# Kernel optimization log

Hardware: AMD Instinct MI355X
Metric: run time of the kernel (lower is better)

## Reference

```python
import jax, jax.numpy as jnp
import numpy as np

EPS = 1e-12  # matches torch F.normalize default eps

def _l2_normalize(v, axis=-1):
    n = jnp.sqrt(jnp.sum(v * v, axis=axis, keepdims=True))
    return v / jnp.maximum(n, EPS)

def setup_inputs() -> dict:
    key = jax.random.key(0)
    k1, k2, k3 = jax.random.split(key, 3)
    B, S, D_IN, D_OUT, T = 4, 4096, 1024, 1024, 1024
    std = 1.0 / np.sqrt(D_IN)
    return {
        "x": jax.random.normal(k1, (B, S, D_IN), dtype=jnp.float32),
        "key_tokens": jax.random.normal(k2, (T, D_IN), dtype=jnp.float32) * std,
        "value_tokens": jax.random.normal(k3, (T, D_OUT), dtype=jnp.float32) * std,
        "temp": jnp.ones((T, 1), dtype=jnp.float32),
    }

def reference(x, key_tokens, value_tokens, temp):
    # x: [B,S,D_in]; key_tokens: [T,D_in]; value_tokens: [T,D_out]; temp: [T,1]
    x_norm = _l2_normalize(x)                      # [B,S,D_in]
    k_norm = _l2_normalize(key_tokens)             # [T,D_in]
    sim = jnp.einsum('bsd,td->bst', x_norm, k_norm)  # [B,S,T]
    sim = sim * jax.nn.sigmoid(temp).reshape(1, 1, -1)
    # mod_softmax: scale each row to RMS-norm sqrt(T), then exact GELU
    T = sim.shape[-1]
    scale = jnp.sqrt(jnp.float32(T)) / jnp.sqrt(jnp.sum(sim * sim, axis=-1, keepdims=True))
    weights = jax.nn.gelu(sim * scale, approximate=False)  # [B,S,T]
    return jnp.einsum('bst,to->bso', weights, value_tokens)  # [B,S,D_out]
```

## Files before the change

### kernel.cpp

```cpp
#include <hip/hip_runtime.h>
#include <math.h>

typedef __attribute__((ext_vector_type(8))) short short8;
typedef __attribute__((ext_vector_type(4))) float floatx4;

__device__ __forceinline__ float bf2f(unsigned short u) {
    union { unsigned int u; float f; } v;
    v.u = ((unsigned int)u) << 16;
    return v.f;
}

__device__ __forceinline__ unsigned short f2bf(float f) {
    union { float f; unsigned int u; } v;
    v.f = f;
    unsigned int r = v.u + 0x7fffu + ((v.u >> 16) & 1u);
    return (unsigned short)(r >> 16);
}

__device__ __forceinline__ void gload16_lds(const void* g, void* l) {
    __builtin_amdgcn_global_load_lds(
        (const __attribute__((address_space(1))) unsigned int*)g,
        (__attribute__((address_space(3))) unsigned int*)l, 16, 0, 0);
}

__global__ __launch_bounds__(256) void prep_kernel(
    const float* __restrict__ x, const float* __restrict__ key,
    const float* __restrict__ temp, const float* __restrict__ val,
    unsigned short* __restrict__ xb, unsigned short* __restrict__ kf,
    unsigned short* __restrict__ VT, float* __restrict__ rowsq,
    int M, int T, int D, int Dout) {
    const int bid = blockIdx.x;
    const int t = threadIdx.x;
    __shared__ float ls[4];
    __shared__ float facs;
    __shared__ unsigned short tile[64][65];

    if (bid < M + T) {
        const bool isx = bid < M;
        const int row = isx ? bid : bid - M;
        const float* src = isx ? (x + (size_t)row * D) : (key + (size_t)row * D);
        float4 v = ((const float4*)src)[t];
        float s = v.x * v.x + v.y * v.y + v.z * v.z + v.w * v.w;
#pragma unroll
        for (int o = 32; o > 0; o >>= 1) s += __shfl_xor(s, o, 64);
        if ((t & 63) == 0) ls[t >> 6] = s;
        __syncthreads();
        if (t == 0) {
            float tot = ls[0] + ls[1] + ls[2] + ls[3];
            float inv = 1.0f / fmaxf(sqrtf(tot), 1e-12f);
            if (isx) {
                facs = inv;
                rowsq[row] = 0.0f;
            } else {
                float tf = temp[row];
                facs = inv / (1.0f + expf(-tf));
            }
        }
        __syncthreads();
        const float fa = facs;
        ushort4 o4;
        o4.x = f2bf(v.x * fa); o4.y = f2bf(v.y * fa);
        o4.z = f2bf(v.z * fa); o4.w = f2bf(v.w * fa);
        unsigned short* dst = isx ? (xb + (size_t)row * D) : (kf + (size_t)row * D);
        ((ushort4*)dst)[t] = o4;
    } else {
        const int idx = bid - M - T;
        const int nCt = Dout >> 6;
        const int c0 = (idx % nCt) * 64;
        const int r0 = (idx / nCt) * 64;
        for (int i = t; i < 4096; i += 256) {
            int r = i >> 6, c = i & 63;
            tile[r][c] = f2bf(val[(size_t)(r0 + r) * Dout + c0 + c]);
        }
        __syncthreads();
        for (int i = t; i < 4096; i += 256) {
            int r = i >> 6, c = i & 63;
            VT[(size_t)(c0 + r) * T + r0 + c] = tile[c][r];
        }
    }
}

template <int MODE>
__global__ __launch_bounds__(256) void gemm_bt(const unsigned short* __restrict__ A,
                                               const unsigned short* __restrict__ B,
                                               void* __restrict__ Cv,
                                               float* __restrict__ rowsq,
                                               int M, int N, int K) {
    __shared__ __align__(16) unsigned short As[128 * 64];
    __shared__ __align__(16) unsigned short Bs[128 * 64];
    const int tid = threadIdx.x;
    const int lane = tid & 63;
    const int w = tid >> 6;
    const int m0 = blockIdx.x * 128;
    const int n0 = blockIdx.y * 128;
    const int wm = (w & 1) * 64;
    const int wn = (w >> 1) * 64;
    const int cl = lane & 15;
    const int q = lane >> 4;

    floatx4 acc[4][4];
#pragma unroll
    for (int i = 0; i < 4; i++)
#pragma unroll
        for (int j = 0; j < 4; j++) acc[i][j] = (floatx4){0.f, 0.f, 0.f, 0.f};

    const int srow = tid >> 2;
    const int skof = (tid & 3) * 8;
    const unsigned short* ga0 = A + (size_t)(m0 + srow) * K + skof;
    const unsigned short* ga1 = A + (size_t)(m0 + srow + 64) * K + skof;
    const unsigned short* gb0 = B + (size_t)(n0 + srow) * K + skof;
    const unsigned short* gb1 = B + (size_t)(n0 + srow + 64) * K + skof;
    unsigned short* la0 = &As[(w * 64) * 8];
    unsigned short* la1 = &As[(256 + w * 64) * 8];
    unsigned short* lb0 = &Bs[(w * 64) * 8];
    unsigned short* lb1 = &Bs[(256 + w * 64) * 8];

    const int a_off = (wm + cl) * 32 + q * 8;
    const int b_off = (wn + cl) * 32 + q * 8;

    for (int kt = 0; kt < K; kt += 64) {
        __syncthreads();
#pragma unroll
        for (int h = 0; h < 2; h++) {
            const int go = kt + h * 32;
            const int lo = h * 4096;
            gload16_lds(ga0 + go, la0 + lo);
            gload16_lds(ga1 + go, la1 + lo);
            gload16_lds(gb0 + go, lb0 + lo);
            gload16_lds(gb1 + go, lb1 + lo);
        }
        __syncthreads();
#pragma unroll
        for (int h = 0; h < 2; h++) {
            const int lo = h * 4096;
            short8 af[4], bfr[4];
#pragma unroll
            for (int mt = 0; mt < 4; mt++)
                af[mt] = *(const short8*)&As[lo + a_off + mt * 16 * 32];
#pragma unroll
            for (int nt = 0; nt < 4; nt++)
                bfr[nt] = *(const short8*)&Bs[lo + b_off + nt * 16 * 32];
#pragma unroll
            for (int mt = 0; mt < 4; mt++)
#pragma unroll
                for (int nt = 0; nt < 4; nt++)
                    acc[mt][nt] = __builtin_amdgcn_mfma_f32_16x16x32_bf16(
                        af[mt], bfr[nt], acc[mt][nt], 0, 0, 0);
        }
    }

#pragma unroll
    for (int mt = 0; mt < 4; mt++) {
#pragma unroll
        for (int r = 0; r < 4; r++) {
            const int m = m0 + wm + mt * 16 + q * 4 + r;
            if (MODE == 0) {
                unsigned short* C = (unsigned short*)Cv;
                float ssq = 0.f;
#pragma unroll
                for (int nt = 0; nt < 4; nt++) {
                    float v = acc[mt][nt][r];
                    ssq += v * v;
                    C[(size_t)m * N + n0 + wn + nt * 16 + cl] = f2bf(v);
                }
#pragma unroll
                for (int o = 1; o < 16; o <<= 1) ssq += __shfl_xor(ssq, o, 64);
                if (cl == 0) atomicAdd(&rowsq[m], ssq);
            } else {
                float* C = (float*)Cv;
#pragma unroll
                for (int nt = 0; nt < 4; nt++)
                    C[(size_t)m * N + n0 + wn + nt * 16 + cl] = acc[mt][nt][r];
            }
        }
    }
}

__global__ __launch_bounds__(256) void gelu_kernel(unsigned short* __restrict__ sim,
                                                   const float* __restrict__ rowsq,
                                                   int T, float sqrtT) {
    const int row = blockIdx.x;
    const float scale = sqrtT / fmaxf(sqrtf(rowsq[row]), 1e-30f);
    ushort4* p = (ushort4*)(sim + (size_t)row * T);
    ushort4 v = p[threadIdx.x];
    float z0 = bf2f(v.x) * scale;
    float z1 = bf2f(v.y) * scale;
    float z2 = bf2f(v.z) * scale;
    float z3 = bf2f(v.w) * scale;
    const float k = 0.70710678118654752f;
    v.x = f2bf(0.5f * z0 * (1.0f + erff(z0 * k)));
    v.y = f2bf(0.5f * z1 * (1.0f + erff(z1 * k)));
    v.z = f2bf(0.5f * z2 * (1.0f + erff(z2 * k)));
    v.w = f2bf(0.5f * z3 * (1.0f + erff(z3 * k)));
    p[threadIdx.x] = v;
}

extern "C" void kernel_launch(void* const* d_in, const int* in_sizes, int n_in,
                              void* d_out, int out_size, void* d_ws, size_t ws_size,
                              hipStream_t stream) {
    const float* x    = (const float*)d_in[0];
    const float* key  = (const float*)d_in[1];
    const float* val  = (const float*)d_in[2];
    const float* temp = (const float*)d_in[3];
    float* out = (float*)d_out;

    const int T = in_sizes[3];
    const int D = in_sizes[1] / T;
    const int Dout = in_sizes[2] / T;
    const int M = in_sizes[0] / D;

    char* ws = (char*)d_ws;
    size_t off = 0;
    unsigned short* xb  = (unsigned short*)(ws + off); off += (size_t)M * D * 2;
    unsigned short* sim = (unsigned short*)(ws + off); off += (size_t)M * T * 2;
    unsigned short* kf  = (unsigned short*)(ws + off); off += (size_t)T * D * 2;
    unsigned short* VT  = (unsigned short*)(ws + off); off += (size_t)Dout * T * 2;
    float* rowsq = (float*)(ws + off); off += (size_t)M * 4;
    (void)ws_size; (void)n_in; (void)out_size;

    const int nTrTiles = (T >> 6) * (Dout >> 6);
    prep_kernel<<<M + T + nTrTiles, 256, 0, stream>>>(x, key, temp, val,
                                                      xb, kf, VT, rowsq, M, T, D, Dout);
    gemm_bt<0><<<dim3(M / 128, T / 128), 256, 0, stream>>>(xb, kf, sim, rowsq, M, T, D);
    gelu_kernel<<<M, 256, 0, stream>>>(sim, rowsq, T, sqrtf((float)T));
    gemm_bt<1><<<dim3(M / 128, Dout / 128), 256, 0, stream>>>(sim, VT, out, nullptr,
                                                              M, Dout, T);
}
```

Measured before the change: 243.1 us.

## Fuse GELU into first GEMM via last-block counter and enlarge GEMM tiles

Removes the separate GELU kernel. Each row-stripe of the first GEMM now keeps a completion counter, and the last block to finish that stripe applies the scale+GELU pass over the whole 256-row strip. Both GEMMs are also retiled to 256x128 with 512 threads, so B tiles are shared across more rows. The cost is that one block per stripe serially processes 256xT elements, a tail on the critical path, in exchange for one fewer launch and less traffic.

```diff
diff --git a/kernel.cpp b/kernel.cpp
--- a/kernel.cpp
+++ b/kernel.cpp
@@ -28,6 +28,7 @@
     const float* __restrict__ temp, const float* __restrict__ val,
     unsigned short* __restrict__ xb, unsigned short* __restrict__ kf,
     unsigned short* __restrict__ VT, float* __restrict__ rowsq,
+    unsigned int* __restrict__ cnt, int nst,
     int M, int T, int D, int Dout) {
     const int bid = blockIdx.x;
     const int t = threadIdx.x;
@@ -51,6 +52,7 @@
             if (isx) {
                 facs = inv;
                 rowsq[row] = 0.0f;
+                if (row < nst) cnt[row] = 0u;
             } else {
                 float tf = temp[row];
                 facs = inv / (1.0f + expf(-tf));
@@ -81,20 +83,23 @@
 }
 
 template <int MODE>
-__global__ __launch_bounds__(256) void gemm_bt(const unsigned short* __restrict__ A,
-                                               const unsigned short* __restrict__ B,
-                                               void* __restrict__ Cv,
-                                               float* __restrict__ rowsq,
-                                               int M, int N, int K) {
-    __shared__ __align__(16) unsigned short As[128 * 64];
-    __shared__ __align__(16) unsigned short Bs[128 * 64];
+__global__ __launch_bounds__(512, 4) void gemm_bt(const unsigned short* __restrict__ A,
+                                                  const unsigned short* __restrict__ B,
+                                                  void* __restrict__ Cv,
+                                                  float* __restrict__ rowsq,
+                                                  unsigned int* __restrict__ cnt,
+                                                  int M, int N, int K,
+                                                  int nblk, float sqrtT, int nshift) {
+    __shared__ __align__(16) unsigned short As[2 * 8192];
+    __shared__ __align__(16) unsigned short Bs[2 * 4096];
+    __shared__ bool sflag;
     const int tid = threadIdx.x;
     const int lane = tid & 63;
     const int w = tid >> 6;
-    const int m0 = blockIdx.x * 128;
+    const int m0 = blockIdx.x * 256;
     const int n0 = blockIdx.y * 128;
-    const int wm = (w & 1) * 64;
-    const int wn = (w >> 1) * 64;
+    const int wm = (w & 3) * 64;
+    const int wn = (w >> 2) * 64;
     const int cl = lane & 15;
     const int q = lane >> 4;
 
@@ -106,14 +111,12 @@
 
     const int srow = tid >> 2;
     const int skof = (tid & 3) * 8;
-    const unsigned short* ga0 = A + (size_t)(m0 + srow) * K + skof;
-    const unsigned short* ga1 = A + (size_t)(m0 + srow + 64) * K + skof;
-    const unsigned short* gb0 = B + (size_t)(n0 + srow) * K + skof;
-    const unsigned short* gb1 = B + (size_t)(n0 + srow + 64) * K + skof;
-    unsigned short* la0 = &As[(w * 64) * 8];
-    unsigned short* la1 = &As[(256 + w * 64) * 8];
-    unsigned short* lb0 = &Bs[(w * 64) * 8];
-    unsigned short* lb1 = &Bs[(256 + w * 64) * 8];
+    const unsigned short* gaA0 = A + (size_t)(m0 + srow) * K + skof;
+    const unsigned short* gaA1 = A + (size_t)(m0 + 128 + srow) * K + skof;
+    const unsigned short* gaB  = B + (size_t)(n0 + srow) * K + skof;
+    unsigned short* ldsA0 = &As[(w * 64) * 8];
+    unsigned short* ldsA1 = &As[4096 + (w * 64) * 8];
+    unsigned short* ldsB  = &Bs[(w * 64) * 8];
 
     const int a_off = (wm + cl) * 32 + q * 8;
     const int b_off = (wn + cl) * 32 + q * 8;
@@ -123,23 +126,22 @@
 #pragma unroll
         for (int h = 0; h < 2; h++) {
             const int go = kt + h * 32;
-            const int lo = h * 4096;
-            gload16_lds(ga0 + go, la0 + lo);
-            gload16_lds(ga1 + go, la1 + lo);
-            gload16_lds(gb0 + go, lb0 + lo);
-            gload16_lds(gb1 + go, lb1 + lo);
+            gload16_lds(gaA0 + go, ldsA0 + h * 8192);
+            gload16_lds(gaA1 + go, ldsA1 + h * 8192);
+            gload16_lds(gaB + go, ldsB + h * 4096);
         }
         __syncthreads();
 #pragma unroll
         for (int h = 0; h < 2; h++) {
-            const int lo = h * 4096;
+            const int ao = h * 8192;
+            const int bo = h * 4096;
             short8 af[4], bfr[4];
 #pragma unroll
             for (int mt = 0; mt < 4; mt++)
-                af[mt] = *(const short8*)&As[lo + a_off + mt * 16 * 32];
+                af[mt] = *(const short8*)&As[ao + a_off + mt * 512];
 #pragma unroll
             for (int nt = 0; nt < 4; nt++)
-                bfr[nt] = *(const short8*)&Bs[lo + b_off + nt * 16 * 32];
+                bfr[nt] = *(const short8*)&Bs[bo + b_off + nt * 512];
 #pragma unroll
             for (int mt = 0; mt < 4; mt++)
 #pragma unroll
@@ -174,25 +176,38 @@
             }
         }
     }
-}
-
-__global__ __launch_bounds__(256) void gelu_kernel(unsigned short* __restrict__ sim,
-                                                   const float* __restrict__ rowsq,
-                                                   int T, float sqrtT) {
-    const int row = blockIdx.x;
-    const float scale = sqrtT / fmaxf(sqrtf(rowsq[row]), 1e-30f);
-    ushort4* p = (ushort4*)(sim + (size_t)row * T);
-    ushort4 v = p[threadIdx.x];
-    float z0 = bf2f(v.x) * scale;
-    float z1 = bf2f(v.y) * scale;
-    float z2 = bf2f(v.z) * scale;
-    float z3 = bf2f(v.w) * scale;
-    const float k = 0.70710678118654752f;
-    v.x = f2bf(0.5f * z0 * (1.0f + erff(z0 * k)));
-    v.y = f2bf(0.5f * z1 * (1.0f + erff(z1 * k)));
-    v.z = f2bf(0.5f * z2 * (1.0f + erff(z2 * k)));
-    v.w = f2bf(0.5f * z3 * (1.0f + erff(z3 * k)));
-    p[threadIdx.x] = v;
+
+    if (MODE == 0) {
+        __threadfence();
+        __syncthreads();
+        if (tid == 0) {
+            unsigned int old = atomicAdd(&cnt[blockIdx.x], 1u);
+            sflag = (old == (unsigned int)(nblk - 1));
+        }
+        __syncthreads();
+        if (sflag) {
+            __threadfence();
+            unsigned short* sim = (unsigned short*)Cv;
+            ushort4* sp = (ushort4*)(sim + (size_t)m0 * N);
+            const int iters = (256 * N) >> 11;
+            const float kk = 0.70710678118654752f;
+            for (int it = 0; it < iters; ++it) {
+                const int f = it * 512 + tid;
+                const int row = m0 + ((unsigned)(f << 2) >> nshift);
+                const float scale = sqrtT / fmaxf(sqrtf(rowsq[row]), 1e-30f);
+                ushort4 v = sp[f];
+                float z0 = bf2f(v.x) * scale;
+                float z1 = bf2f(v.y) * scale;
+                float z2 = bf2f(v.z) * scale;
+                float z3 = bf2f(v.w) * scale;
+                v.x = f2bf(0.5f * z0 * (1.0f + erff(z0 * kk)));
+                v.y = f2bf(0.5f * z1 * (1.0f + erff(z1 * kk)));
+                v.z = f2bf(0.5f * z2 * (1.0f + erff(z2 * kk)));
+                v.w = f2bf(0.5f * z3 * (1.0f + erff(z3 * kk)));
+                sp[f] = v;
+            }
+        }
+    }
 }
 
 extern "C" void kernel_launch(void* const* d_in, const int* in_sizes, int n_in,
@@ -216,13 +231,20 @@
     unsigned short* kf  = (unsigned short*)(ws + off); off += (size_t)T * D * 2;
     unsigned short* VT  = (unsigned short*)(ws + off); off += (size_t)Dout * T * 2;
     float* rowsq = (float*)(ws + off); off += (size_t)M * 4;
+    unsigned int* cnt = (unsigned int*)(ws + off); off += (size_t)(M / 256) * 4;
     (void)ws_size; (void)n_in; (void)out_size;
 
+    const int nst = M / 256;
+    int nshift = 0;
+    while ((1 << nshift) < T) nshift++;
+
     const int nTrTiles = (T >> 6) * (Dout >> 6);
-    prep_kernel<<<M + T + nTrTiles, 256, 0, stream>>>(x, key, temp, val,
-                                                      xb, kf, VT, rowsq, M, T, D, Dout);
-    gemm_bt<0><<<dim3(M / 128, T / 128), 256, 0, stream>>>(xb, kf, sim, rowsq, M, T, D);
-    gelu_kernel<<<M, 256, 0, stream>>>(sim, rowsq, T, sqrtf((float)T));
-    gemm_bt<1><<<dim3(M / 128, Dout / 128), 256, 0, stream>>>(sim, VT, out, nullptr,
-                                                              M, Dout, T);
-}
+    prep_kernel<<<M + T + nTrTiles, 256, 0, stream>>>(x, key, temp, val, xb, kf, VT,
+                                                      rowsq, cnt, nst, M, T, D, Dout);
+    gemm_bt<0><<<dim3(M / 256, T / 128), 512, 0, stream>>>(xb, kf, sim, rowsq, cnt,
+                                                           M, T, D, T / 128,
+                                                           sqrtf((float)T), nshift);
+    gemm_bt<1><<<dim3(M / 256, Dout / 128), 512, 0, stream>>>(sim, VT, out, nullptr,
+                                                              nullptr, M, Dout, T,
+                                                              0, 0.f, 0);
+}
```

Result: slower. 438.1 us (+80.2%).
